# Optimization experiments

Hardware: AMD Instinct MI355X
Metric: run time of the kernel (lower is better)

Reference implementation:

```python
import jax, jax.numpy as jnp
import numpy as np

DIMS = 1024
HEADS = 16
DEPTH = DIMS // HEADS


def setup_inputs() -> dict:
    key = jax.random.key(0)
    kq, kk, kv = jax.random.split(key, 3)
    B, S = 2, 2048
    q = jax.random.normal(kq, (B, S, DIMS), dtype=jnp.float32)
    k = jax.random.normal(kk, (B, S, DIMS), dtype=jnp.float32)
    v = jax.random.normal(kv, (B, S, DIMS), dtype=jnp.float32)
    return {"q": q, "k": k, "v": v}


def _split_heads(x):
    # [B, S, dims] -> [B, heads, S, depth]
    b, s, _ = x.shape
    return x.reshape(b, s, HEADS, DEPTH).transpose(0, 2, 1, 3)


def reference(q, k, v):
    b, s, _ = q.shape
    qh = _split_heads(q)  # [b, h, sq, d]
    kh = _split_heads(k)  # [b, h, sk, d]
    vh = _split_heads(v)  # [b, h, sk, d]
    # keras.layers.Attention default: UNSCALED dot-product scores
    scores = jnp.einsum("bhqd,bhkd->bhqk", qh, kh)
    weights = jax.nn.softmax(scores, axis=-1)
    out = jnp.einsum("bhqk,bhkd->bhqd", weights, vh)
    # merge heads: [b, h, sq, d] -> [b, sq, dims]
    out = out.transpose(0, 2, 1, 3).reshape(b, s, DIMS)
    return out
```

## Files before the change

kernel.cpp:

```cpp
#include <hip/hip_runtime.h>

#define SEQ 2048
#define HEADS 16
#define DEPTH 64
#define DIMS 1024
#define LOG2E 1.44269504088896340736f
#define NTILES 64

typedef _Float16 f16x8 __attribute__((ext_vector_type(8)));
typedef __fp16 fp16v2 __attribute__((ext_vector_type(2)));
typedef float f32x16 __attribute__((ext_vector_type(16)));

__device__ __forceinline__ f32x16 mfma32(f16x8 a, f16x8 b, f32x16 c) {
  return __builtin_amdgcn_mfma_f32_32x32x16_f16(a, b, c, 0, 0, 0);
}

#if __has_builtin(__builtin_amdgcn_exp2f)
#define EXP2(x) __builtin_amdgcn_exp2f(x)
#else
#define EXP2(x) exp2f(x)
#endif

__device__ __forceinline__ unsigned pkbits(float a, float b) {
  union { fp16v2 h; unsigned u; } cv;
  cv.h = __builtin_amdgcn_cvt_pkrtz(a, b);
  return cv.u;
}

#define GLOAD_LDS(g, l)                                                        \
  __builtin_amdgcn_global_load_lds(                                            \
      (const __attribute__((address_space(1))) unsigned int*)(g),              \
      (__attribute__((address_space(3))) unsigned int*)(l), 16, 0, 0)

#define WAITC(n)                                                               \
  do {                                                                         \
    asm volatile("s_waitcnt vmcnt(" #n ")" ::: "memory");                      \
    __builtin_amdgcn_sched_barrier(0);                                         \
  } while (0)

__global__ __launch_bounds__(256) void prep_kv(const float* __restrict__ k,
                                               const float* __restrict__ v,
                                               _Float16* __restrict__ khf,
                                               _Float16* __restrict__ vtp) {
  const int bid = blockIdx.x;
  if (bid < 2048) {
    int t = bid * 256 + threadIdx.x;
    size_t flat = (size_t)t * 8;
    int b = (int)(flat >> 21);
    int rem = (int)(flat & ((1u << 21) - 1));
    int s = rem >> 10;
    int c = rem & 1023;
    int h = c >> 6;
    int d = c & 63;
    float4 a0 = *(const float4*)(k + flat);
    float4 a1 = *(const float4*)(k + flat + 4);
    float f[8] = {a0.x, a0.y, a0.z, a0.w, a1.x, a1.y, a1.z, a1.w};
    f16x8 th;
    #pragma unroll
    for (int j = 0; j < 8; ++j) th[j] = (_Float16)f[j];
    size_t o = ((size_t)(b * HEADS + h) * SEQ + s) * DEPTH + d;
    *(f16x8*)(khf + o) = th;
  } else {
    int t = (bid - 2048) * 256 + threadIdx.x;
    int d = t & 63;
    int sg = (t >> 6) & 255;
    int bh = t >> 14;
    int b = bh >> 4, h = bh & 15;
    int s0 = sg * 8;
    const float* src = v + ((size_t)(b * SEQ + s0)) * DIMS + h * DEPTH + d;
    _Float16* dst = vtp + ((size_t)bh * DEPTH + d) * SEQ + s0;
    f16x8 tv;
    #pragma unroll
    for (int i = 0; i < 8; ++i) tv[i] = (_Float16)src[(size_t)i * DIMS];
    *(f16x8*)dst = tv;
  }
}

__global__ __launch_bounds__(256, 2) void attn_fwd(
    const float* __restrict__ q, const _Float16* __restrict__ kh,
    const _Float16* __restrict__ vt, float* __restrict__ out) {
  __shared__ _Float16 lds[4][2][4096];

  const int tid = threadIdx.x;
  const int w = tid >> 6;
  const int l = tid & 63;
  const int q32 = l & 31;
  const int hi = l >> 5;

  const int bid = blockIdx.x;
  const int wg = (bid & 7) * 64 + (bid >> 3);
  const int qt = wg & 15;
  const int bh = wg >> 4;
  const int b = bh >> 4;
  const int h = bh & 15;

  const int qb = qt * 128 + w * 32;
  const int hoff = h * DEPTH;
  const size_t kvoff = (size_t)bh * SEQ * DEPTH;

  f16x8 qf[4];
  {
    const float* gq = q + (size_t)(b * SEQ + qb + q32) * DIMS + hoff + 8 * hi;
    #pragma unroll
    for (int c = 0; c < 4; ++c) {
      float4 a0 = *(const float4*)(gq + 16 * c);
      float4 a1 = *(const float4*)(gq + 16 * c + 4);
      float f[8] = {a0.x, a0.y, a0.z, a0.w, a1.x, a1.y, a1.z, a1.w};
      f16x8 t;
      #pragma unroll
      for (int j = 0; j < 8; ++j) t[j] = (_Float16)(f[j] * LOG2E);
      qf[c] = t;
    }
  }

  const int j8 = l >> 3;
  const int j4 = l >> 2;
  const _Float16* gkp[4];
  const _Float16* gvp[4];
  #pragma unroll
  for (int i = 0; i < 4; ++i) {
    gkp[i] = kh + kvoff + (size_t)(8 * i + j8) * DEPTH +
             (((l & 7) ^ j8 ^ (i & 3)) * 8);
    gvp[i] = vt + kvoff + (size_t)(16 * i + (j4 & 15)) * SEQ +
             (((l & 3) ^ (j4 & 3)) * 8);
  }

  const int kmask = (q32 & 7) ^ ((q32 >> 3) & 3);
  int koff[4];
  #pragma unroll
  for (int c = 0; c < 4; ++c) koff[c] = q32 * 64 + ((2 * c + hi) ^ kmask) * 8;
  const int vmask = q32 & 3;
  int voff0[2], voff1[2];
  #pragma unroll
  for (int s = 0; s < 2; ++s) {
    const int ch = (2 * s + hi) ^ vmask;
    voff0[s] = 2048 + q32 * 32 + ch * 8;
    voff1[s] = 2048 + (32 + q32) * 32 + ch * 8;
  }

  f32x16 acc0 = {}, acc1 = {};
  f32x16 dacc = {};
  float mrow = -3e38f;

  const f16x8 onesf = {1, 1, 1, 1, 1, 1, 1, 1};

  auto stage = [&](int buf, int t) {
    _Float16* base = &lds[w][buf][0];
    #pragma unroll
    for (int i = 0; i < 4; ++i)
      GLOAD_LDS(gkp[i] + (size_t)t * 32 * DEPTH, base + i * 512);
    #pragma unroll
    for (int i = 0; i < 4; ++i)
      GLOAD_LDS(gvp[i] + t * 32, base + 2048 + i * 512);
  };

  auto compute = [&](int buf) {
    const _Float16* base = &lds[w][buf][0];
    f32x16 st = {};
    __builtin_amdgcn_s_setprio(1);
    #pragma unroll
    for (int c = 0; c < 4; ++c) {
      f16x8 kf = *(const f16x8*)(base + koff[c]);
      st = mfma32(kf, qf[c], st);
    }
    __builtin_amdgcn_s_setprio(0);

    float mx = fmaxf(st[0], st[1]);
    #pragma unroll
    for (int r = 2; r < 16; ++r) mx = fmaxf(mx, st[r]);
    if (!__all(mx - mrow <= 8.0f)) {
      mx = fmaxf(mx, __shfl_xor(mx, 32));
      float mnew = fmaxf(mrow, mx);
      float sc = EXP2(mrow - mnew);
      mrow = mnew;
      #pragma unroll
      for (int r = 0; r < 16; ++r) {
        const int crow = (r & 3) + 8 * (r >> 2) + 4 * hi;
        float scb = __shfl(sc, crow);
        acc0[r] *= scb;
        acc1[r] *= scb;
        dacc[r] *= scb;
      }
    }
    #pragma unroll
    for (int r = 0; r < 16; ++r) st[r] = EXP2(st[r] - mrow);

    f16x8 pa[2];
    #pragma unroll
    for (int sl = 0; sl < 2; ++sl) {
      unsigned x0 = pkbits(st[8 * sl + 0], st[8 * sl + 1]);
      unsigned x1 = pkbits(st[8 * sl + 2], st[8 * sl + 3]);
      unsigned y0 = pkbits(st[8 * sl + 4], st[8 * sl + 5]);
      unsigned y1 = pkbits(st[8 * sl + 6], st[8 * sl + 7]);
      asm("v_permlane32_swap_b32 %0, %1" : "+v"(x0), "+v"(y0));
      asm("v_permlane32_swap_b32 %0, %1" : "+v"(x1), "+v"(y1));
      union { unsigned u[4]; f16x8 v; } pu;
      pu.u[0] = x0; pu.u[1] = x1; pu.u[2] = y0; pu.u[3] = y1;
      pa[sl] = pu.v;
    }

    __builtin_amdgcn_s_setprio(1);
    #pragma unroll
    for (int s = 0; s < 2; ++s) {
      f16x8 vf0 = *(const f16x8*)(base + voff0[s]);
      f16x8 vf1 = *(const f16x8*)(base + voff1[s]);
      acc0 = mfma32(pa[s], vf0, acc0);
      acc1 = mfma32(pa[s], vf1, acc1);
      dacc = mfma32(pa[s], onesf, dacc);
    }
    __builtin_amdgcn_s_setprio(0);
  };

  stage(0, 0);
  #pragma unroll 1
  for (int t = 0; t < NTILES; t += 2) {
    stage(1, t + 1);
    WAITC(8);
    compute(0);
    if (t + 2 < NTILES) {
      stage(0, t + 2);
      WAITC(8);
    } else {
      WAITC(0);
    }
    compute(1);
  }

  #pragma unroll
  for (int r = 0; r < 16; ++r) {
    const int crow = (r & 3) + 8 * (r >> 2) + 4 * hi;
    float rden = 1.0f / dacc[r];
    float* po = out + (size_t)(b * SEQ + qb + crow) * DIMS + hoff;
    po[q32] = acc0[r] * rden;
    po[32 + q32] = acc1[r] * rden;
  }
}

extern "C" void kernel_launch(void* const* d_in, const int* in_sizes, int n_in,
                              void* d_out, int out_size, void* d_ws, size_t ws_size,
                              hipStream_t stream) {
  const float* q = (const float*)d_in[0];
  const float* k = (const float*)d_in[1];
  const float* v = (const float*)d_in[2];
  float* out = (float*)d_out;

  const size_t tsz = (size_t)2 * HEADS * SEQ * DEPTH;
  _Float16* khf = (_Float16*)d_ws;
  _Float16* vtp = khf + tsz;

  prep_kv<<<4096, 256, 0, stream>>>(k, v, khf, vtp);
  attn_fwd<<<512, 256, 0, stream>>>(q, khf, vtp, out);
}
```

Before: 81.37 us.

## Share 128-key K/V tiles across waves via block-wide LDS staging

Before, each of the four waves staged its own private 32-key K/V tiles in LDS, so the same data was loaded from global memory four times per block. Now the whole block loads 128-key K and V tiles cooperatively into shared LDS buffers, and every wave computes four 32x32 score blocks per tile. Manual vmcnt waits are replaced with block-wide __syncthreads barriers, which keeps double buffering but adds synchronisation across waves. Larger per-iteration score tiles also mean fewer softmax max/rescale checks per key, at the cost of more live registers.

```diff
diff --git a/kernel.cpp b/kernel.cpp
--- a/kernel.cpp
+++ b/kernel.cpp
@@ -5,7 +5,7 @@
 #define DEPTH 64
 #define DIMS 1024
 #define LOG2E 1.44269504088896340736f
-#define NTILES 64
+#define NT128 16
 
 typedef _Float16 f16x8 __attribute__((ext_vector_type(8)));
 typedef __fp16 fp16v2 __attribute__((ext_vector_type(2)));
@@ -31,12 +31,6 @@
   __builtin_amdgcn_global_load_lds(                                            \
       (const __attribute__((address_space(1))) unsigned int*)(g),              \
       (__attribute__((address_space(3))) unsigned int*)(l), 16, 0, 0)
-
-#define WAITC(n)                                                               \
-  do {                                                                         \
-    asm volatile("s_waitcnt vmcnt(" #n ")" ::: "memory");                      \
-    __builtin_amdgcn_sched_barrier(0);                                         \
-  } while (0)
 
 __global__ __launch_bounds__(256) void prep_kv(const float* __restrict__ k,
                                                const float* __restrict__ v,
@@ -79,7 +73,8 @@
 __global__ __launch_bounds__(256, 2) void attn_fwd(
     const float* __restrict__ q, const _Float16* __restrict__ kh,
     const _Float16* __restrict__ vt, float* __restrict__ out) {
-  __shared__ _Float16 lds[4][2][4096];
+  __shared__ _Float16 Kl[2][128 * 64];
+  __shared__ _Float16 Vl[2][64 * 128];
 
   const int tid = threadIdx.x;
   const int w = tid >> 6;
@@ -113,30 +108,24 @@
     }
   }
 
-  const int j8 = l >> 3;
-  const int j4 = l >> 2;
   const _Float16* gkp[4];
   const _Float16* gvp[4];
   #pragma unroll
   for (int i = 0; i < 4; ++i) {
-    gkp[i] = kh + kvoff + (size_t)(8 * i + j8) * DEPTH +
-             (((l & 7) ^ j8 ^ (i & 3)) * 8);
-    gvp[i] = vt + kvoff + (size_t)(16 * i + (j4 & 15)) * SEQ +
-             (((l & 3) ^ (j4 & 3)) * 8);
-  }
-
-  const int kmask = (q32 & 7) ^ ((q32 >> 3) & 3);
-  int koff[4];
-  #pragma unroll
-  for (int c = 0; c < 4; ++c) koff[c] = q32 * 64 + ((2 * c + hi) ^ kmask) * 8;
-  const int vmask = q32 & 3;
-  int voff0[2], voff1[2];
-  #pragma unroll
-  for (int s = 0; s < 2; ++s) {
-    const int ch = (2 * s + hi) ^ vmask;
-    voff0[s] = 2048 + q32 * 32 + ch * 8;
-    voff1[s] = 2048 + (32 + q32) * 32 + ch * 8;
-  }
+    const int krow = 32 * w + 8 * i + (l >> 3);
+    gkp[i] = kh + kvoff + (size_t)krow * DEPTH +
+             (((l & 7) ^ (l >> 3) ^ ((4 * w + i) & 3)) * 8);
+    const int vrow = 16 * w + 4 * i + (l >> 4);
+    const int vmask = (vrow & 7) ^ ((vrow >> 3) & 3);
+    gvp[i] = vt + kvoff + (size_t)vrow * SEQ + (((l & 15) ^ vmask) * 8);
+  }
+
+  const int mask0 = (q32 & 7) ^ ((q32 >> 3) & 3);
+  int kco[4], vco[8];
+  #pragma unroll
+  for (int c = 0; c < 4; ++c) kco[c] = ((2 * c + hi) ^ mask0) * 8;
+  #pragma unroll
+  for (int s = 0; s < 8; ++s) vco[s] = ((2 * s + hi) ^ mask0) * 8;
 
   f32x16 acc0 = {}, acc1 = {};
   f32x16 dacc = {};
@@ -145,29 +134,36 @@
   const f16x8 onesf = {1, 1, 1, 1, 1, 1, 1, 1};
 
   auto stage = [&](int buf, int t) {
-    _Float16* base = &lds[w][buf][0];
     #pragma unroll
     for (int i = 0; i < 4; ++i)
-      GLOAD_LDS(gkp[i] + (size_t)t * 32 * DEPTH, base + i * 512);
+      GLOAD_LDS(gkp[i] + (size_t)t * 128 * DEPTH,
+                &Kl[buf][(32 * w + 8 * i) * 64]);
     #pragma unroll
     for (int i = 0; i < 4; ++i)
-      GLOAD_LDS(gvp[i] + t * 32, base + 2048 + i * 512);
+      GLOAD_LDS(gvp[i] + t * 128, &Vl[buf][(16 * w + 4 * i) * 128]);
   };
 
   auto compute = [&](int buf) {
-    const _Float16* base = &lds[w][buf][0];
-    f32x16 st = {};
+    f32x16 st[4];
     __builtin_amdgcn_s_setprio(1);
     #pragma unroll
-    for (int c = 0; c < 4; ++c) {
-      f16x8 kf = *(const f16x8*)(base + koff[c]);
-      st = mfma32(kf, qf[c], st);
+    for (int k = 0; k < 4; ++k) {
+      f32x16 z = {};
+      st[k] = z;
+      #pragma unroll
+      for (int c = 0; c < 4; ++c) {
+        f16x8 kf = *(const f16x8*)&Kl[buf][(32 * k + q32) * 64 + kco[c]];
+        st[k] = mfma32(kf, qf[c], st[k]);
+      }
     }
     __builtin_amdgcn_s_setprio(0);
 
-    float mx = fmaxf(st[0], st[1]);
-    #pragma unroll
-    for (int r = 2; r < 16; ++r) mx = fmaxf(mx, st[r]);
+    float mx = fmaxf(st[0][0], st[0][1]);
+    #pragma unroll
+    for (int k = 0; k < 4; ++k)
+      #pragma unroll
+      for (int r = (k == 0 ? 2 : 0); r < 16; r += 2)
+        mx = fmaxf(mx, fmaxf(st[k][r], st[k][r + 1]));
     if (!__all(mx - mrow <= 8.0f)) {
       mx = fmaxf(mx, __shfl_xor(mx, 32));
       float mnew = fmaxf(mrow, mx);
@@ -183,27 +179,32 @@
       }
     }
     #pragma unroll
-    for (int r = 0; r < 16; ++r) st[r] = EXP2(st[r] - mrow);
-
-    f16x8 pa[2];
-    #pragma unroll
-    for (int sl = 0; sl < 2; ++sl) {
-      unsigned x0 = pkbits(st[8 * sl + 0], st[8 * sl + 1]);
-      unsigned x1 = pkbits(st[8 * sl + 2], st[8 * sl + 3]);
-      unsigned y0 = pkbits(st[8 * sl + 4], st[8 * sl + 5]);
-      unsigned y1 = pkbits(st[8 * sl + 6], st[8 * sl + 7]);
-      asm("v_permlane32_swap_b32 %0, %1" : "+v"(x0), "+v"(y0));
-      asm("v_permlane32_swap_b32 %0, %1" : "+v"(x1), "+v"(y1));
-      union { unsigned u[4]; f16x8 v; } pu;
-      pu.u[0] = x0; pu.u[1] = x1; pu.u[2] = y0; pu.u[3] = y1;
-      pa[sl] = pu.v;
+    for (int k = 0; k < 4; ++k)
+      #pragma unroll
+      for (int r = 0; r < 16; ++r) st[k][r] = EXP2(st[k][r] - mrow);
+
+    f16x8 pa[8];
+    #pragma unroll
+    for (int k = 0; k < 4; ++k) {
+      #pragma unroll
+      for (int sl = 0; sl < 2; ++sl) {
+        unsigned x0 = pkbits(st[k][8 * sl + 0], st[k][8 * sl + 1]);
+        unsigned x1 = pkbits(st[k][8 * sl + 2], st[k][8 * sl + 3]);
+        unsigned y0 = pkbits(st[k][8 * sl + 4], st[k][8 * sl + 5]);
+        unsigned y1 = pkbits(st[k][8 * sl + 6], st[k][8 * sl + 7]);
+        asm("v_permlane32_swap_b32 %0, %1" : "+v"(x0), "+v"(y0));
+        asm("v_permlane32_swap_b32 %0, %1" : "+v"(x1), "+v"(y1));
+        union { unsigned u[4]; f16x8 v; } pu;
+        pu.u[0] = x0; pu.u[1] = x1; pu.u[2] = y0; pu.u[3] = y1;
+        pa[2 * k + sl] = pu.v;
+      }
     }
 
     __builtin_amdgcn_s_setprio(1);
     #pragma unroll
-    for (int s = 0; s < 2; ++s) {
-      f16x8 vf0 = *(const f16x8*)(base + voff0[s]);
-      f16x8 vf1 = *(const f16x8*)(base + voff1[s]);
+    for (int s = 0; s < 8; ++s) {
+      f16x8 vf0 = *(const f16x8*)&Vl[buf][q32 * 128 + vco[s]];
+      f16x8 vf1 = *(const f16x8*)&Vl[buf][(32 + q32) * 128 + vco[s]];
       acc0 = mfma32(pa[s], vf0, acc0);
       acc1 = mfma32(pa[s], vf1, acc1);
       dacc = mfma32(pa[s], onesf, dacc);
@@ -212,18 +213,15 @@
   };
 
   stage(0, 0);
+  __syncthreads();
   #pragma unroll 1
-  for (int t = 0; t < NTILES; t += 2) {
+  for (int t = 0; t < NT128; t += 2) {
     stage(1, t + 1);
-    WAITC(8);
     compute(0);
-    if (t + 2 < NTILES) {
-      stage(0, t + 2);
-      WAITC(8);
-    } else {
-      WAITC(0);
-    }
+    __syncthreads();
+    if (t + 2 < NT128) stage(0, t + 2);
     compute(1);
+    __syncthreads();
   }
 
   #pragma unroll
```

Measured after the change: 67.33 us, median of 2. -17.3%, faster.
